# Kernel tuning notes

Hardware: AMD Instinct MI355X
Metric: run time of the kernel (lower is better)

Reference implementation:

```python
import jax, jax.numpy as jnp
import numpy as np

B, Y = 1024, 50000
MAX_TRIALS = 4096


def setup_inputs() -> dict:
    key = jax.random.key(0)
    k1, k2 = jax.random.split(key)
    input_ = jax.random.normal(k1, (B, Y), dtype=jnp.float32)
    pos = jax.random.randint(k2, (B,), 0, Y)
    target = jnp.zeros((B, Y), jnp.float32).at[jnp.arange(B), pos].set(1.0)
    return {"input_": input_, "target": target, "max_num_trials": MAX_TRIALS}


def reference(input_, target, max_num_trials):
    """WARP loss. The torch original sequentially samples negatives WITHOUT
    replacement per row until margin 1 + s_neg - s_pos >= 0 or max_num_trials
    is hit. Sampling without replacement == taking a uniform random
    permutation of the negative labels and scanning it; the first violating
    position t gives num_trials = t+1. This lets us fully vectorize the
    irregular loop while computing identical math (up to RNG stream)."""
    Bn, Yn = input_.shape
    rows = jnp.arange(Bn)
    pos = jnp.argmax(target, axis=1)                 # one positive per row (as J[i,1])
    pos_score = input_[rows, pos]                    # [B]

    # uniform random permutation of the Y-1 negatives per row:
    # random sort keys, force the positive label to sort last, drop it.
    u = jax.random.uniform(jax.random.key(42), (Bn, Yn))
    u = u.at[rows, pos].set(2.0)
    perm = jnp.argsort(u, axis=1)[:, : Yn - 1]       # [B, Y-1] negative label ids

    neg_scores = jnp.take_along_axis(input_, perm, axis=1)   # [B, Y-1]
    margins = 1.0 + neg_scores - pos_score[:, None]
    trial_ok = jnp.arange(Yn - 1)[None, :] < max_num_trials
    viol = (margins >= 0.0) & trial_ok
    found = jnp.any(viol, axis=1)
    first = jnp.argmax(viol, axis=1)                 # first violating trial index
    num_trials = (first + 1).astype(jnp.float32)
    # loss_weight = log(floor((Y-1)/num_trials)); 0 when no violator found
    L = jnp.where(found, jnp.log(jnp.floor((Yn - 1.0) / num_trials)), 0.0)
    neg_score = jnp.where(
        found, jnp.take_along_axis(neg_scores, first[:, None], axis=1)[:, 0], 0.0
    )
    loss = L * (1.0 - pos_score + neg_score)         # [B]
    return jnp.sum(loss, keepdims=True)              # shape (1,), as torch.sum(dim=0, keepdim=True)
```

## Files before the change

### kernel.cpp

```cpp
#include <hip/hip_runtime.h>
#include <stdint.h>

#define BN 1024
#define YN 50000
#define SEGS 8
#define SEGLEN 6250
#define CAP_BIG 1024
#define CAP_SMALL 192
#define LCAP 256

#if defined(__has_builtin)
#  if __has_builtin(__builtin_amdgcn_alignbit)
#    define ROTL(x, r) __builtin_amdgcn_alignbit((x), (x), 32u - (r))
#  endif
#endif
#ifndef ROTL
#  define ROTL(x, r) (((x) << (r)) | ((x) >> (32 - (r))))
#endif

#define TFR(r) { x0 += x1; x1 = ROTL(x1, r) ^ x0; }

__device__ __forceinline__ uint32_t tf_core(uint32_t v) {
    const uint32_t ks1 = 42u;
    const uint32_t ks2 = 0x1BD11BDAu ^ 42u;
    uint32_t x0 = v;
    uint32_t x1 = (ROTL(v, 13u)) ^ v;
    TFR(15u) TFR(26u) TFR(6u)
    x0 += ks1; x1 += ks2 + 1u;
    TFR(17u) TFR(29u) TFR(16u) TFR(24u)
    x0 += ks2; x1 += 2u;
    TFR(13u) TFR(15u) TFR(26u) TFR(6u)
     x1 += ks1 + 3u;
    TFR(17u) TFR(29u) TFR(16u) TFR(24u)
    x0 += ks1; x1 += ks2 + 4u;
    TFR(13u) TFR(15u) TFR(26u) TFR(6u)
    x0 += ks2; x1 += 5u;
    return x0 ^ x1;
}

struct WS {
    uint32_t* cnt; uint32_t* done; int* pos; float* ps; float* row_loss; uint32_t* cand;
};
static inline WS ws_layout(void* d_ws) {
    uint32_t* p = (uint32_t*)d_ws;
    WS w;
    w.cnt = p; w.done = p + BN; w.pos = (int*)(p + 2 * BN);
    w.ps = (float*)(p + 3 * BN); w.row_loss = (float*)(p + 4 * BN);
    w.cand = p + 5 * BN;
    return w;
}

__global__ __launch_bounds__(256) void gen_kernel(
    const float* __restrict__ input, const float* __restrict__ target,
    uint32_t* __restrict__ cnt, uint32_t* __restrict__ cand,
    int* __restrict__ pos_out, float* __restrict__ ps_out,
    uint32_t thr, int cap)
{
    const int tid = threadIdx.x;
    if (blockIdx.x < BN) {
        const int row = blockIdx.x;
        const size_t base = (size_t)row * YN;
        __shared__ volatile int s_pos;
        if (tid == 0) s_pos = -1;
        __syncthreads();
        const float4* t4 = (const float4*)(target + base);
        for (int j4 = tid; j4 < YN / 4; j4 += 256) {
            if (s_pos >= 0) break;
            float4 v = t4[j4];
            int c0 = 4 * j4;
            if (v.x != 0.0f) s_pos = c0;
            if (v.y != 0.0f) s_pos = c0 + 1;
            if (v.z != 0.0f) s_pos = c0 + 2;
            if (v.w != 0.0f) s_pos = c0 + 3;
        }
        __syncthreads();
        if (tid == 0) {
            int p = s_pos;
            pos_out[row] = p;
            ps_out[row] = input[base + p];
        }
        return;
    }
    const int b = blockIdx.x - BN;
    const int row = b >> 3;
    const int seg = b & 7;
    const uint32_t base32 = (uint32_t)row * YN;
    const int start = seg * SEGLEN;

    __shared__ uint32_t s_buf[LCAP];
    __shared__ uint32_t s_cnt;
    __shared__ uint32_t s_base;
    if (tid == 0) s_cnt = 0;
    __syncthreads();

    int col = start + tid;
    uint32_t cb = base32 + (uint32_t)col;
    for (int k = 0; k < 6; ++k) {
        uint32_t b0 = tf_core(cb + 42u);
        uint32_t b1 = tf_core(cb + 298u);
        uint32_t b2 = tf_core(cb + 554u);
        uint32_t b3 = tf_core(cb + 810u);
        if (b0 < thr) {
            uint32_t i = atomicAdd(&s_cnt, 1u);
            if (i < LCAP) s_buf[i] = ((b0 >> 9) << 16) | (uint32_t)col;
        }
        if (b1 < thr) {
            uint32_t i = atomicAdd(&s_cnt, 1u);
            if (i < LCAP) s_buf[i] = ((b1 >> 9) << 16) | (uint32_t)(col + 256);
        }
        if (b2 < thr) {
            uint32_t i = atomicAdd(&s_cnt, 1u);
            if (i < LCAP) s_buf[i] = ((b2 >> 9) << 16) | (uint32_t)(col + 512);
        }
        if (b3 < thr) {
            uint32_t i = atomicAdd(&s_cnt, 1u);
            if (i < LCAP) s_buf[i] = ((b3 >> 9) << 16) | (uint32_t)(col + 768);
        }
        col += 1024; cb += 1024u;
    }
    if (tid < SEGLEN - 6144) {
        uint32_t bt = tf_core(cb + 42u);
        if (bt < thr) {
            uint32_t i = atomicAdd(&s_cnt, 1u);
            if (i < LCAP) s_buf[i] = ((bt >> 9) << 16) | (uint32_t)col;
        }
    }
    __syncthreads();

    const uint32_t tot = s_cnt;
    if (tid == 0) {
        if (tot > LCAP) {
            atomicAdd(cnt + row, 1u << 20);
            s_base = 0xFFFFFFFFu;
        } else {
            s_base = atomicAdd(cnt + row, tot);
        }
    }
    __syncthreads();
    const uint32_t base_ = s_base;
    if (base_ != 0xFFFFFFFFu) {
        uint32_t* mycand = cand + (size_t)row * (size_t)cap;
        for (uint32_t i = tid; i < tot; i += 256) {
            uint32_t gi = base_ + i;
            if (gi < (uint32_t)cap) mycand[gi] = s_buf[i];
        }
    }
}

__global__ __launch_bounds__(256) void finish_kernel(
    const float* __restrict__ input, const uint32_t* __restrict__ cnt,
    const uint32_t* __restrict__ cand, const int* __restrict__ pos_,
    const float* __restrict__ ps_, const int* __restrict__ mt_ptr,
    float* __restrict__ row_loss, uint32_t* __restrict__ done,
    float* __restrict__ out, int cap)
{
    const int tid = threadIdx.x;
    const int wid = tid >> 6;
    const int lane = tid & 63;
    const int row = blockIdx.x * 4 + wid;
    const int pos = pos_[row];
    const float ps = ps_[row];
    const float* rowp = input + (size_t)row * YN;
    const uint32_t n = cnt[row];
    const uint32_t mt = (uint32_t)mt_ptr[0];

    __shared__ int s_fb[4];
    __shared__ uint64_t s_min64[256];
    __shared__ uint32_t s_sum[256];

    float loss = 0.0f;
    bool need_fallback = (n > (uint32_t)cap);

    if (!need_fallback) {
        const uint32_t* cl = cand + (size_t)row * (size_t)cap;
        uint32_t mk = 0xFFFFFFFFu;
        for (uint32_t i = lane; i < n; i += 64) {
            uint32_t e = cl[i];
            int col = (int)(e & 0xFFFFu);
            if (col != pos) {
                float s = rowp[col];
                if ((1.0f + s) - ps >= 0.0f) mk = (e < mk) ? e : mk;
            }
        }
        for (int off = 32; off > 0; off >>= 1) {
            uint32_t o = (uint32_t)__shfl_xor((int)mk, off, 64);
            mk = (o < mk) ? o : mk;
        }
        if (mk == 0xFFFFFFFFu) {
            need_fallback = true;
        } else {
            uint32_t c = 0;
            for (uint32_t i = lane; i < n; i += 64) {
                uint32_t e = cl[i];
                int col = (int)(e & 0xFFFFu);
                c += ((e < mk) && (col != pos)) ? 1u : 0u;
            }
            for (int off = 32; off > 0; off >>= 1)
                c += (uint32_t)__shfl_xor((int)c, off, 64);
            if (c < mt) {
                int cstar = (int)(mk & 0xFFFFu);
                float ns = rowp[cstar];
                float nt = (float)(c + 1u);
                loss = logf(floorf(49999.0f / nt)) * ((1.0f - ps) + ns);
            }
        }
    }
    if (lane == 0) {
        s_fb[wid] = need_fallback ? row : -1;
        if (!need_fallback) row_loss[row] = loss;
    }
    __syncthreads();

    for (int w = 0; w < 4; ++w) {
        const int frow = s_fb[w];
        if (frow < 0) continue;
        const int fpos = pos_[frow];
        const float fps = ps_[frow];
        const float* frp = input + (size_t)frow * YN;
        const uint32_t fb32 = (uint32_t)frow * YN;
        uint64_t mk64 = ~0ull;
        for (int col = tid; col < YN; col += 256) {
            uint32_t bits = tf_core(fb32 + (uint32_t)col + 42u);
            uint64_t key = ((uint64_t)(bits >> 9) << 16) | (uint32_t)col;
            float m = (1.0f + frp[col]) - fps;
            if ((m >= 0.0f) && (col != fpos) && (key < mk64)) mk64 = key;
        }
        s_min64[tid] = mk64;
        __syncthreads();
        for (int s = 128; s > 0; s >>= 1) {
            if (tid < s) { uint64_t o = s_min64[tid + s]; if (o < s_min64[tid]) s_min64[tid] = o; }
            __syncthreads();
        }
        const uint64_t kstar = s_min64[0];
        __syncthreads();
        if (kstar == ~0ull) {
            if (tid == 0) row_loss[frow] = 0.0f;
            continue;
        }
        uint32_t c = 0;
        for (int col = tid; col < YN; col += 256) {
            uint32_t bits = tf_core(fb32 + (uint32_t)col + 42u);
            uint64_t key = ((uint64_t)(bits >> 9) << 16) | (uint32_t)col;
            c += ((key < kstar) && (col != fpos)) ? 1u : 0u;
        }
        s_sum[tid] = c;
        __syncthreads();
        for (int s = 128; s > 0; s >>= 1) {
            if (tid < s) s_sum[tid] += s_sum[tid + s];
            __syncthreads();
        }
        if (tid == 0) {
            uint32_t rank = s_sum[0];
            float fl = 0.0f;
            if (rank < mt) {
                int cstar = (int)(kstar & 0xFFFFull);
                float ns = frp[cstar];
                float nt = (float)(rank + 1u);
                fl = logf(floorf(49999.0f / nt)) * ((1.0f - fps) + ns);
            }
            row_loss[frow] = fl;
        }
        __syncthreads();
    }

    __threadfence();
    __syncthreads();
    __shared__ bool s_last;
    if (tid == 0) s_last = (atomicAdd(done, 1u) == (uint32_t)(gridDim.x - 1));
    __syncthreads();
    if (s_last) {
        __threadfence();
        __shared__ float s[256];
        float acc = 0.0f;
        for (int i = tid; i < BN; i += 256) acc += row_loss[i];
        s[tid] = acc;
        __syncthreads();
        for (int st = 128; st > 0; st >>= 1) {
            if (tid < st) s[tid] += s[tid + st];
            __syncthreads();
        }
        if (tid == 0) out[0] = s[0];
    }
}

extern "C" void kernel_launch(void* const* d_in, const int* in_sizes, int n_in,
                              void* d_out, int out_size, void* d_ws, size_t ws_size,
                              hipStream_t stream) {
    const float* input  = (const float*)d_in[0];
    const float* target = (const float*)d_in[1];
    const int*   mt     = (const int*)d_in[2];
    float* out = (float*)d_out;
    WS w = ws_layout(d_ws);

    const size_t need_big = (size_t)(5 * BN) * 4 + (size_t)BN * CAP_BIG * 4;
    uint32_t thr; int cap;
    if (ws_size >= need_big) { thr = 1u << 25; cap = CAP_BIG; }
    else                     { thr = 1u << 23; cap = CAP_SMALL; }

    hipMemsetAsync(d_ws, 0, 2 * BN * sizeof(uint32_t), stream);

    gen_kernel<<<BN + BN * SEGS, 256, 0, stream>>>(
        input, target, w.cnt, w.cand, w.pos, w.ps, thr, cap);
    finish_kernel<<<BN / 4, 256, 0, stream>>>(
        input, w.cnt, w.cand, w.pos, w.ps, mt, w.row_loss, w.done, out, cap);
}
```

Measured before the change: 453.2 us.

## Fuse candidate generation and per-row resolve into one kernel via per-row tickets

```diff
diff --git a/kernel.cpp b/kernel.cpp
--- a/kernel.cpp
+++ b/kernel.cpp
@@ -39,26 +39,148 @@
 }
 
 struct WS {
-    uint32_t* cnt; uint32_t* done; int* pos; float* ps; float* row_loss; uint32_t* cand;
+    uint32_t* cnt; uint32_t* ready; uint32_t* done;
+    int* pos; float* ps; float* row_loss; uint32_t* cand;
 };
 static inline WS ws_layout(void* d_ws) {
     uint32_t* p = (uint32_t*)d_ws;
     WS w;
-    w.cnt = p; w.done = p + BN; w.pos = (int*)(p + 2 * BN);
-    w.ps = (float*)(p + 3 * BN); w.row_loss = (float*)(p + 4 * BN);
-    w.cand = p + 5 * BN;
+    w.cnt = p; w.ready = p + BN; w.done = p + 2 * BN;
+    w.pos = (int*)(p + 3 * BN); w.ps = (float*)(p + 4 * BN);
+    w.row_loss = (float*)(p + 5 * BN);
+    w.cand = p + 6 * BN;
     return w;
 }
 
-__global__ __launch_bounds__(256) void gen_kernel(
+__device__ void block_resolve(
+    int row, int tid, const float* __restrict__ input,
+    const uint32_t* __restrict__ cnt, const uint32_t* __restrict__ cand,
+    const int* __restrict__ pos_, const float* __restrict__ ps_,
+    uint32_t mt, float* __restrict__ row_loss, int cap,
+    uint32_t* s_u32, uint64_t* s_u64)
+{
+    const uint32_t n = cnt[row];
+    const int pos = pos_[row];
+    const float ps = ps_[row];
+    const float* rowp = input + (size_t)row * YN;
+    bool fb = (n > (uint32_t)cap);
+
+    if (!fb) {
+        const uint32_t* cl = cand + (size_t)row * (size_t)cap;
+        uint32_t mk = 0xFFFFFFFFu;
+        for (uint32_t i = tid; i < n; i += 256) {
+            uint32_t e = cl[i];
+            int col = (int)(e & 0xFFFFu);
+            if (col != pos) {
+                float s = rowp[col];
+                if ((1.0f + s) - ps >= 0.0f) mk = (e < mk) ? e : mk;
+            }
+        }
+        s_u32[tid] = mk;
+        __syncthreads();
+        for (int st = 128; st > 0; st >>= 1) {
+            if (tid < st) { uint32_t o = s_u32[tid + st]; if (o < s_u32[tid]) s_u32[tid] = o; }
+            __syncthreads();
+        }
+        mk = s_u32[0];
+        __syncthreads();
+        if (mk == 0xFFFFFFFFu) {
+            fb = true;
+        } else {
+            uint32_t c = 0;
+            for (uint32_t i = tid; i < n; i += 256) {
+                uint32_t e = cl[i];
+                int col = (int)(e & 0xFFFFu);
+                c += ((e < mk) && (col != pos)) ? 1u : 0u;
+            }
+            s_u32[tid] = c;
+            __syncthreads();
+            for (int st = 128; st > 0; st >>= 1) {
+                if (tid < st) s_u32[tid] += s_u32[tid + st];
+                __syncthreads();
+            }
+            if (tid == 0) {
+                uint32_t rank = s_u32[0];
+                float loss = 0.0f;
+                if (rank < mt) {
+                    int cstar = (int)(mk & 0xFFFFu);
+                    float ns = rowp[cstar];
+                    float nt = (float)(rank + 1u);
+                    loss = logf(floorf(49999.0f / nt)) * ((1.0f - ps) + ns);
+                }
+                row_loss[row] = loss;
+            }
+            __syncthreads();
+        }
+    }
+    if (fb) {
+        const uint32_t fb32 = (uint32_t)row * YN;
+        uint64_t mk64 = ~0ull;
+        for (int col = tid; col < YN; col += 256) {
+            uint32_t bits = tf_core(fb32 + (uint32_t)col + 42u);
+            uint64_t key = ((uint64_t)(bits >> 9) << 16) | (uint32_t)col;
+            float m = (1.0f + rowp[col]) - ps;
+            if ((m >= 0.0f) && (col != pos) && (key < mk64)) mk64 = key;
+        }
+        s_u64[tid] = mk64;
+        __syncthreads();
+        for (int st = 128; st > 0; st >>= 1) {
+            if (tid < st) { uint64_t o = s_u64[tid + st]; if (o < s_u64[tid]) s_u64[tid] = o; }
+            __syncthreads();
+        }
+        const uint64_t kstar = s_u64[0];
+        __syncthreads();
+        if (kstar == ~0ull) {
+            if (tid == 0) row_loss[row] = 0.0f;
+        } else {
+            uint32_t c = 0;
+            for (int col = tid; col < YN; col += 256) {
+                uint32_t bits = tf_core(fb32 + (uint32_t)col + 42u);
+                uint64_t key = ((uint64_t)(bits >> 9) << 16) | (uint32_t)col;
+                c += ((key < kstar) && (col != pos)) ? 1u : 0u;
+            }
+            s_u32[tid] = c;
+            __syncthreads();
+            for (int st = 128; st > 0; st >>= 1) {
+                if (tid < st) s_u32[tid] += s_u32[tid + st];
+                __syncthreads();
+            }
+            if (tid == 0) {
+                uint32_t rank = s_u32[0];
+                float fl = 0.0f;
+                if (rank < mt) {
+                    int cstar = (int)(kstar & 0xFFFFull);
+                    float ns = rowp[cstar];
+                    float nt = (float)(rank + 1u);
+                    fl = logf(floorf(49999.0f / nt)) * ((1.0f - ps) + ns);
+                }
+                row_loss[row] = fl;
+            }
+        }
+        __syncthreads();
+    }
+}
+
+__global__ __launch_bounds__(256) void warp_kernel(
     const float* __restrict__ input, const float* __restrict__ target,
-    uint32_t* __restrict__ cnt, uint32_t* __restrict__ cand,
+    uint32_t* __restrict__ cnt, uint32_t* __restrict__ ready,
+    uint32_t* __restrict__ done, uint32_t* __restrict__ cand,
     int* __restrict__ pos_out, float* __restrict__ ps_out,
-    uint32_t thr, int cap)
+    const int* __restrict__ mt_ptr, float* __restrict__ row_loss,
+    float* __restrict__ out, uint32_t thr, int cap)
 {
     const int tid = threadIdx.x;
+    int myrow;
+
+    __shared__ uint32_t s_buf[LCAP];
+    __shared__ uint32_t s_cnt, s_base;
+    __shared__ uint32_t s_u32[256];
+    __shared__ uint64_t s_u64[256];
+    __shared__ uint32_t s_tkt;
+
     if (blockIdx.x < BN) {
         const int row = blockIdx.x;
+        myrow = row;
         const size_t base = (size_t)row * YN;
         __shared__ volatile int s_pos;
         if (tid == 0) s_pos = -1;
@@ -79,208 +201,102 @@
             pos_out[row] = p;
             ps_out[row] = input[base + p];
         }
-        return;
-    }
-    const int b = blockIdx.x - BN;
-    const int row = b >> 3;
-    const int seg = b & 7;
-    const uint32_t base32 = (uint32_t)row * YN;
-    const int start = seg * SEGLEN;
-
-    __shared__ uint32_t s_buf[LCAP];
-    __shared__ uint32_t s_cnt;
-    __shared__ uint32_t s_base;
-    if (tid == 0) s_cnt = 0;
-    __syncthreads();
-
-    int col = start + tid;
-    uint32_t cb = base32 + (uint32_t)col;
-    for (int k = 0; k < 6; ++k) {
-        uint32_t b0 = tf_core(cb + 42u);
-        uint32_t b1 = tf_core(cb + 298u);
-        uint32_t b2 = tf_core(cb + 554u);
-        uint32_t b3 = tf_core(cb + 810u);
-        if (b0 < thr) {
-            uint32_t i = atomicAdd(&s_cnt, 1u);
-            if (i < LCAP) s_buf[i] = ((b0 >> 9) << 16) | (uint32_t)col;
-        }
-        if (b1 < thr) {
-            uint32_t i = atomicAdd(&s_cnt, 1u);
-            if (i < LCAP) s_buf[i] = ((b1 >> 9) << 16) | (uint32_t)(col + 256);
-        }
-        if (b2 < thr) {
-            uint32_t i = atomicAdd(&s_cnt, 1u);
-            if (i < LCAP) s_buf[i] = ((b2 >> 9) << 16) | (uint32_t)(col + 512);
-        }
-        if (b3 < thr) {
-            uint32_t i = atomicAdd(&s_cnt, 1u);
-            if (i < LCAP) s_buf[i] = ((b3 >> 9) << 16) | (uint32_t)(col + 768);
-        }
-        col += 1024; cb += 1024u;
-    }
-    if (tid < SEGLEN - 6144) {
-        uint32_t bt = tf_core(cb + 42u);
-        if (bt < thr) {
-            uint32_t i = atomicAdd(&s_cnt, 1u);
-            if (i < LCAP) s_buf[i] = ((bt >> 9) << 16) | (uint32_t)col;
-        }
-    }
-    __syncthreads();
-
-    const uint32_t tot = s_cnt;
+    } else {
+        const int b = blockIdx.x - BN;
+        const int row = b >> 3;
+        myrow = row;
+        const int seg = b & 7;
+        const uint32_t base32 = (uint32_t)row * YN;
+        const int start = seg * SEGLEN;
+        if (tid == 0) s_cnt = 0;
+        __syncthreads();
+
+        int col = start + tid;
+        uint32_t cb = base32 + (uint32_t)col;
+        for (int k = 0; k < 6; ++k) {
+            uint32_t b0 = tf_core(cb + 42u);
+            uint32_t b1 = tf_core(cb + 298u);
+            uint32_t b2 = tf_core(cb + 554u);
+            uint32_t b3 = tf_core(cb + 810u);
+            if (b0 < thr) {
+                uint32_t i = atomicAdd(&s_cnt, 1u);
+                if (i < LCAP) s_buf[i] = ((b0 >> 9) << 16) | (uint32_t)col;
+            }
+            if (b1 < thr) {
+                uint32_t i = atomicAdd(&s_cnt, 1u);
+                if (i < LCAP) s_buf[i] = ((b1 >> 9) << 16) | (uint32_t)(col + 256);
+            }
+            if (b2 < thr) {
+                uint32_t i = atomicAdd(&s_cnt, 1u);
+                if (i < LCAP) s_buf[i] = ((b2 >> 9) << 16) | (uint32_t)(col + 512);
+            }
+            if (b3 < thr) {
+                uint32_t i = atomicAdd(&s_cnt, 1u);
+                if (i < LCAP) s_buf[i] = ((b3 >> 9) << 16) | (uint32_t)(col + 768);
+            }
+            col += 1024; cb += 1024u;
+        }
+        if (tid < SEGLEN - 6144) {
+            uint32_t bt = tf_core(cb + 42u);
+            if (bt < thr) {
+                uint32_t i = atomicAdd(&s_cnt, 1u);
+                if (i < LCAP) s_buf[i] = ((bt >> 9) << 16) | (uint32_t)col;
+            }
+        }
+        __syncthreads();
+
+        const uint32_t tot = s_cnt;
+        if (tid == 0) {
+            if (tot > LCAP) {
+                atomicAdd(cnt + row, 1u << 20);
+                s_base = 0xFFFFFFFFu;
+            } else {
+                s_base = atomicAdd(cnt + row, tot);
+            }
+        }
+        __syncthreads();
+        const uint32_t base_ = s_base;
+        if (base_ != 0xFFFFFFFFu) {
+            uint32_t* mycand = cand + (size_t)row * (size_t)cap;
+            for (uint32_t i = tid; i < tot; i += 256) {
+                uint32_t gi = base_ + i;
+                if (gi < (uint32_t)cap) mycand[gi] = s_buf[i];
+            }
+        }
+    }
+
+    __syncthreads();
     if (tid == 0) {
-        if (tot > LCAP) {
-            atomicAdd(cnt + row, 1u << 20);
-            s_base = 0xFFFFFFFFu;
-        } else {
-            s_base = atomicAdd(cnt + row, tot);
-        }
-    }
-    __syncthreads();
-    const uint32_t base_ = s_base;
-    if (base_ != 0xFFFFFFFFu) {
-        uint32_t* mycand = cand + (size_t)row * (size_t)cap;
-        for (uint32_t i = tid; i < tot; i += 256) {
-            uint32_t gi = base_ + i;
-            if (gi < (uint32_t)cap) mycand[gi] = s_buf[i];
-        }
-    }
-}
-
-__global__ __launch_bounds__(256) void finish_kernel(
-    const float* __restrict__ input, const uint32_t* __restrict__ cnt,
-    const uint32_t* __restrict__ cand, const int* __restrict__ pos_,
-    const float* __restrict__ ps_, const int* __restrict__ mt_ptr,
-    float* __restrict__ row_loss, uint32_t* __restrict__ done,
-    float* __restrict__ out, int cap)
-{
-    const int tid = threadIdx.x;
-    const int wid = tid >> 6;
-    const int lane = tid & 63;
-    const int row = blockIdx.x * 4 + wid;
-    const int pos = pos_[row];
-    const float ps = ps_[row];
-    const float* rowp = input + (size_t)row * YN;
-    const uint32_t n = cnt[row];
+        __threadfence();
+        s_tkt = atomicAdd(ready + myrow, 1u);
+    }
+    __syncthreads();
+    if (s_tkt != SEGS) return;
+
+    __threadfence();
     const uint32_t mt = (uint32_t)mt_ptr[0];
-
-    __shared__ int s_fb[4];
-    __shared__ uint64_t s_min64[256];
-    __shared__ uint32_t s_sum[256];
-
-    float loss = 0.0f;
-    bool need_fallback = (n > (uint32_t)cap);
-
-    if (!need_fallback) {
-        const uint32_t* cl = cand + (size_t)row * (size_t)cap;
-        uint32_t mk = 0xFFFFFFFFu;
-        for (uint32_t i = lane; i < n; i += 64) {
-            uint32_t e = cl[i];
-            int col = (int)(e & 0xFFFFu);
-            if (col != pos) {
-                float s = rowp[col];
-                if ((1.0f + s) - ps >= 0.0f) mk = (e < mk) ? e : mk;
-            }
-        }
-        for (int off = 32; off > 0; off >>= 1) {
-            uint32_t o = (uint32_t)__shfl_xor((int)mk, off, 64);
-            mk = (o < mk) ? o : mk;
-        }
-        if (mk == 0xFFFFFFFFu) {
-            need_fallback = true;
-        } else {
-            uint32_t c = 0;
-            for (uint32_t i = lane; i < n; i += 64) {
-                uint32_t e = cl[i];
-                int col = (int)(e & 0xFFFFu);
-                c += ((e < mk) && (col != pos)) ? 1u : 0u;
-            }
-            for (int off = 32; off > 0; off >>= 1)
-                c += (uint32_t)__shfl_xor((int)c, off, 64);
-            if (c < mt) {
-                int cstar = (int)(mk & 0xFFFFu);
-                float ns = rowp[cstar];
-                float nt = (float)(c + 1u);
-                loss = logf(floorf(49999.0f / nt)) * ((1.0f - ps) + ns);
-            }
-        }
-    }
-    if (lane == 0) {
-        s_fb[wid] = need_fallback ? row : -1;
-        if (!need_fallback) row_loss[row] = loss;
-    }
-    __syncthreads();
-
-    for (int w = 0; w < 4; ++w) {
-        const int frow = s_fb[w];
-        if (frow < 0) continue;
-        const int fpos = pos_[frow];
-        const float fps = ps_[frow];
-        const float* frp = input + (size_t)frow * YN;
-        const uint32_t fb32 = (uint32_t)frow * YN;
-        uint64_t mk64 = ~0ull;
-        for (int col = tid; col < YN; col += 256) {
-            uint32_t bits = tf_core(fb32 + (uint32_t)col + 42u);
-            uint64_t key = ((uint64_t)(bits >> 9) << 16) | (uint32_t)col;
-            float m = (1.0f + frp[col]) - fps;
-            if ((m >= 0.0f) && (col != fpos) && (key < mk64)) mk64 = key;
-        }
-        s_min64[tid] = mk64;
-        __syncthreads();
-        for (int s = 128; s > 0; s >>= 1) {
-            if (tid < s) { uint64_t o = s_min64[tid + s]; if (o < s_min64[tid]) s_min64[tid] = o; }
-            __syncthreads();
-        }
-        const uint64_t kstar = s_min64[0];
-        __syncthreads();
-        if (kstar == ~0ull) {
-            if (tid == 0) row_loss[frow] = 0.0f;
-            continue;
-        }
-        uint32_t c = 0;
-        for (int col = tid; col < YN; col += 256) {
-            uint32_t bits = tf_core(fb32 + (uint32_t)col + 42u);
-            uint64_t key = ((uint64_t)(bits >> 9) << 16) | (uint32_t)col;
-            c += ((key < kstar) && (col != fpos)) ? 1u : 0u;
-        }
-        s_sum[tid] = c;
-        __syncthreads();
-        for (int s = 128; s > 0; s >>= 1) {
-            if (tid < s) s_sum[tid] += s_sum[tid + s];
-            __syncthreads();
-        }
-        if (tid == 0) {
-            uint32_t rank = s_sum[0];
-            float fl = 0.0f;
-            if (rank < mt) {
-                int cstar = (int)(kstar & 0xFFFFull);
-                float ns = frp[cstar];
-                float nt = (float)(rank + 1u);
-                fl = logf(floorf(49999.0f / nt)) * ((1.0f - fps) + ns);
-            }
-            row_loss[frow] = fl;
-        }
-        __syncthreads();
-    }
+    block_resolve(myrow, tid, input, cnt, cand, pos_out, ps_out,
+                  mt, row_loss, cap, s_u32, s_u64);
+
+    __syncthreads();
+    if (tid == 0) {
+        __threadfence();
+        s_tkt = atomicAdd(done, 1u);
+    }
+    __syncthreads();
+    if (s_tkt != (uint32_t)(BN - 1)) return;
 
     __threadfence();
-    __syncthreads();
-    __shared__ bool s_last;
-    if (tid == 0) s_last = (atomicAdd(done, 1u) == (uint32_t)(gridDim.x - 1));
-    __syncthreads();
-    if (s_last) {
-        __threadfence();
-        __shared__ float s[256];
-        float acc = 0.0f;
-        for (int i = tid; i < BN; i += 256) acc += row_loss[i];
-        s[tid] = acc;
-        __syncthreads();
-        for (int st = 128; st > 0; st >>= 1) {
-            if (tid < st) s[tid] += s[tid + st];
-            __syncthreads();
-        }
-        if (tid == 0) out[0] = s[0];
-    }
+    __shared__ float s[256];
+    float acc = 0.0f;
+    for (int i = tid; i < BN; i += 256) acc += row_loss[i];
+    s[tid] = acc;
+    __syncthreads();
+    for (int st = 128; st > 0; st >>= 1) {
+        if (tid < st) s[tid] += s[tid + st];
+        __syncthreads();
+    }
+    if (tid == 0) out[0] = s[0];
 }
 
 extern "C" void kernel_launch(void* const* d_in, const int* in_sizes, int n_in,
@@ -292,15 +308,14 @@
     float* out = (float*)d_out;
     WS w = ws_layout(d_ws);
 
-    const size_t need_big = (size_t)(5 * BN) * 4 + (size_t)BN * CAP_BIG * 4;
+    const size_t need_big = (size_t)(6 * BN) * 4 + (size_t)BN * CAP_BIG * 4;
     uint32_t thr; int cap;
     if (ws_size >= need_big) { thr = 1u << 25; cap = CAP_BIG; }
     else                     { thr = 1u << 23; cap = CAP_SMALL; }
 
-    hipMemsetAsync(d_ws, 0, 2 * BN * sizeof(uint32_t), stream);
-
-    gen_kernel<<<BN + BN * SEGS, 256, 0, stream>>>(
-        input, target, w.cnt, w.cand, w.pos, w.ps, thr, cap);
-    finish_kernel<<<BN / 4, 256, 0, stream>>>(
-        input, w.cnt, w.cand, w.pos, w.ps, mt, w.row_loss, w.done, out, cap);
-}
+    hipMemsetAsync(d_ws, 0, 3 * BN * sizeof(uint32_t), stream);
+
+    warp_kernel<<<BN + BN * SEGS, 256, 0, stream>>>(
+        input, target, w.cnt, w.ready, w.done, w.cand,
+        w.pos, w.ps, mt, w.row_loss, out, thr, cap);
+}
```

Result: slower. 1.551 ms (+242.3%).
